# Kernel optimization log

Measured on AMD Instinct MI355X. Metric: run time of the kernel, lower is better.

## Reference

```python
import jax, jax.numpy as jnp
import numpy as np

DIM = 768
HEADS = 12
DIM_HEAD = DIM // HEADS  # 64
INNER = DIM_HEAD * HEADS  # 768
HIDDEN = 4 * DIM  # 3072
N = 31  # num_patches + 1, fixed by Block (num_patches=30)
B = 512
EPS = 1e-5
MASK_VAL = -987654321.0


def layernorm(x, g, b):
    mu = jnp.mean(x, axis=-1, keepdims=True)
    var = jnp.mean(jnp.square(x - mu), axis=-1, keepdims=True)
    return (x - mu) * jax.lax.rsqrt(var + EPS) * g + b


def setup_inputs() -> dict:
    key = jax.random.key(0)
    ks = jax.random.split(key, 12)
    s = 0.02
    return {
        "x": jax.random.normal(ks[0], (B, N, DIM), jnp.float32),
        "ln1_g": jnp.ones((DIM,), jnp.float32),
        "ln1_b": jnp.zeros((DIM,), jnp.float32),
        "w_qkv": jax.random.normal(ks[1], (DIM, 3 * INNER), jnp.float32) * s,
        "scale": jnp.full((HEADS,), DIM_HEAD ** -0.5, jnp.float32),
        "w_o": jax.random.normal(ks[2], (INNER, DIM), jnp.float32) * s,
        "b_o": jnp.zeros((DIM,), jnp.float32),
        "ln2_g": jnp.ones((DIM,), jnp.float32),
        "ln2_b": jnp.zeros((DIM,), jnp.float32),
        "w1": jax.random.normal(ks[3], (DIM, HIDDEN), jnp.float32) * s,
        "b1": jnp.zeros((HIDDEN,), jnp.float32),
        "w2": jax.random.normal(ks[4], (HIDDEN, DIM), jnp.float32) * s,
        "b2": jnp.zeros((DIM,), jnp.float32),
    }


def reference(x, ln1_g, ln1_b, w_qkv, scale, w_o, b_o, ln2_g, ln2_b, w1, b1, w2, b2):
    b, n, _ = x.shape
    # --- LSA attention ---
    h = layernorm(x, ln1_g, ln1_b)
    qkv = h @ w_qkv  # [b, n, 3*inner]
    q, k, v = jnp.split(qkv, 3, axis=-1)
    def split_heads(t):
        return t.reshape(b, n, HEADS, DIM_HEAD).transpose(0, 2, 1, 3)  # b h n d
    q, k, v = split_heads(q), split_heads(k), split_heads(v)
    dots = jnp.einsum('bhid,bhjd->bhij', q, k) * scale[None, :, None, None]
    # diagonal exclusion mask (self-token masked out)
    diag = jnp.eye(n, dtype=bool)
    dots = jnp.where(diag[None, None], MASK_VAL, dots)
    attn = jax.nn.softmax(dots, axis=-1)
    out = jnp.einsum('bhij,bhjd->bhid', attn, v)
    out = out.transpose(0, 2, 1, 3).reshape(b, n, INNER)
    x = x + out @ w_o + b_o
    # --- MLP ---
    h2 = layernorm(x, ln2_g, ln2_b)
    h2 = jax.nn.gelu(h2 @ w1 + b1, approximate=False)
    x = x + h2 @ w2 + b2
    return x
```

## Files before the change

### kernel.cpp

```cpp
#include <hip/hip_runtime.h>
#include <math.h>

#define DIM 768
#define HEADS 12
#define DHEAD 64
#define NTOK 31
#define BATCH 512
#define MTOK (BATCH * NTOK)
#define HIDDEN 3072
#define QKVN 2304
#define MASK_VAL -987654321.0f

typedef short s16x8 __attribute__((ext_vector_type(8)));
typedef float f32x4 __attribute__((ext_vector_type(4)));

static __device__ __forceinline__ float bs2f(unsigned short u) {
  unsigned int x = ((unsigned int)u) << 16;
  return __builtin_bit_cast(float, x);
}
static __device__ __forceinline__ unsigned short f2bs(float f) {
  unsigned int x = __builtin_bit_cast(unsigned int, f);
  x += 0x7fffu + ((x >> 16) & 1u);
  return (unsigned short)(x >> 16);
}

static __device__ __forceinline__ void gload16(const unsigned short* g, unsigned short* l) {
  __builtin_amdgcn_global_load_lds(
      (const __attribute__((address_space(1))) unsigned int*)g,
      (__attribute__((address_space(3))) unsigned int*)l, 16, 0, 0);
}

static __device__ __forceinline__ float epi_apply(int EPI, float v, int col, size_t idx,
                                                  const float* bias, const void* resid) {
  if (EPI == 0) return v;
  if (EPI == 2) {
    float t = v + bias[col];
    float arg = 1.5957691216f * t * (1.f + 0.044715f * t * t);
    return t * __builtin_amdgcn_rcpf(1.f + __expf(-arg));
  }
  if (EPI == 3) return v + bias[col] + ((const float*)resid)[idx];
  return v + bias[col] + bs2f(((const unsigned short*)resid)[idx]);
}

static __device__ __forceinline__ void epi_store(int EPI, void* outp, size_t idx, float t) {
  if (EPI == 4) ((float*)outp)[idx] = t;
  else ((unsigned short*)outp)[idx] = f2bs(t);
}

__global__ __launch_bounds__(256) void transpose_all_kernel(
    const float* __restrict__ w_qkv, const float* __restrict__ w_o,
    const float* __restrict__ w1, const float* __restrict__ w2,
    unsigned short* __restrict__ wqkvT, unsigned short* __restrict__ woT,
    unsigned short* __restrict__ w1T, unsigned short* __restrict__ w2T) {
  int t = blockIdx.x;
  const float* w;
  unsigned short* wt;
  int K, N, tx;
  if (t < 432) { w = w_qkv; wt = wqkvT; K = DIM; N = QKVN; tx = QKVN / 64; }
  else if (t < 576) { t -= 432; w = w_o; wt = woT; K = DIM; N = DIM; tx = DIM / 64; }
  else if (t < 1152) { t -= 576; w = w1; wt = w1T; K = DIM; N = HIDDEN; tx = HIDDEN / 64; }
  else { t -= 1152; w = w2; wt = w2T; K = HIDDEN; N = DIM; tx = DIM / 64; }
  int n0 = (t % tx) * 64, k0 = (t / tx) * 64;

  __shared__ float tl[64][65];
  int tid = threadIdx.x;
  int r = tid >> 4, c4 = (tid & 15) * 4;
#pragma unroll
  for (int i = 0; i < 4; ++i) {
    float4 v = *(const float4*)(w + (size_t)(k0 + r + i * 16) * N + n0 + c4);
    tl[r + i * 16][c4] = v.x;
    tl[r + i * 16][c4 + 1] = v.y;
    tl[r + i * 16][c4 + 2] = v.z;
    tl[r + i * 16][c4 + 3] = v.w;
  }
  __syncthreads();
#pragma unroll
  for (int i = 0; i < 4; ++i) {
    int n = r + i * 16;
    ushort4 o;
    o.x = f2bs(tl[c4 + 0][n]);
    o.y = f2bs(tl[c4 + 1][n]);
    o.z = f2bs(tl[c4 + 2][n]);
    o.w = f2bs(tl[c4 + 3][n]);
    *(ushort4*)(wt + (size_t)(n0 + n) * K + k0 + c4) = o;
  }
}

__global__ __launch_bounds__(256) void ln_kernel(const float* __restrict__ x,
                                                 const float* __restrict__ g,
                                                 const float* __restrict__ bta,
                                                 unsigned short* __restrict__ out) {
  int wid = threadIdx.x >> 6, lane = threadIdx.x & 63;
  size_t row = (size_t)blockIdx.x * 4 + wid;
  const float4* xr = (const float4*)(x + row * DIM);
  float4 v[3];
  v[0] = xr[lane];
  v[1] = xr[lane + 64];
  v[2] = xr[lane + 128];
  float s = 0.f, sq = 0.f;
#pragma unroll
  for (int i = 0; i < 3; ++i) {
    s += v[i].x + v[i].y + v[i].z + v[i].w;
    sq += v[i].x * v[i].x + v[i].y * v[i].y + v[i].z * v[i].z + v[i].w * v[i].w;
  }
#pragma unroll
  for (int off = 32; off; off >>= 1) {
    s += __shfl_xor(s, off);
    sq += __shfl_xor(sq, off);
  }
  float mu = s * (1.f / DIM);
  float var = sq * (1.f / DIM) - mu * mu;
  float rs = rsqrtf(var + 1e-5f);
#pragma unroll
  for (int i = 0; i < 3; ++i) {
    int col = i * 256 + lane * 4;
    float4 gg = *(const float4*)(g + col);
    float4 bb = *(const float4*)(bta + col);
    ushort4 o;
    o.x = f2bs((v[i].x - mu) * rs * gg.x + bb.x);
    o.y = f2bs((v[i].y - mu) * rs * gg.y + bb.y);
    o.z = f2bs((v[i].z - mu) * rs * gg.z + bb.z);
    o.w = f2bs((v[i].w - mu) * rs * gg.w + bb.w);
    *(ushort4*)(out + row * DIM + col) = o;
  }
}

__global__ __launch_bounds__(256) void ln_bf16_kernel(const unsigned short* __restrict__ x,
                                                      const float* __restrict__ g,
                                                      const float* __restrict__ bta,
                                                      unsigned short* __restrict__ out) {
  int wid = threadIdx.x >> 6, lane = threadIdx.x & 63;
  size_t row = (size_t)blockIdx.x * 4 + wid;
  const unsigned short* xr = x + row * DIM;
  float v[12];
#pragma unroll
  for (int i = 0; i < 3; ++i) {
    ushort4 u = *(const ushort4*)(xr + i * 256 + lane * 4);
    v[i * 4 + 0] = bs2f(u.x);
    v[i * 4 + 1] = bs2f(u.y);
    v[i * 4 + 2] = bs2f(u.z);
    v[i * 4 + 3] = bs2f(u.w);
  }
  float s = 0.f, sq = 0.f;
#pragma unroll
  for (int i = 0; i < 12; ++i) {
    s += v[i];
    sq += v[i] * v[i];
  }
#pragma unroll
  for (int off = 32; off; off >>= 1) {
    s += __shfl_xor(s, off);
    sq += __shfl_xor(sq, off);
  }
  float mu = s * (1.f / DIM);
  float var = sq * (1.f / DIM) - mu * mu;
  float rs = rsqrtf(var + 1e-5f);
#pragma unroll
  for (int i = 0; i < 3; ++i) {
    int col = i * 256 + lane * 4;
    float4 gg = *(const float4*)(g + col);
    float4 bb = *(const float4*)(bta + col);
    ushort4 o;
    o.x = f2bs((v[i * 4 + 0] - mu) * rs * gg.x + bb.x);
    o.y = f2bs((v[i * 4 + 1] - mu) * rs * gg.y + bb.y);
    o.z = f2bs((v[i * 4 + 2] - mu) * rs * gg.z + bb.z);
    o.w = f2bs((v[i * 4 + 3] - mu) * rs * gg.w + bb.w);
    *(ushort4*)(out + row * DIM + col) = o;
  }
}

template <int AB, int BB, int VM, typename STF>
__device__ __forceinline__ void gphm(const char* aBase, const char* bBase,
                                     f32x4 (&acc)[4][4], STF&& stage) {
  const char* aP = aBase + AB * 8192;
  const char* bP = bBase + BB * 16384;
  s16x8 af[4], bk[4];
#pragma unroll
  for (int ni = 0; ni < 4; ++ni) bk[ni] = *(const s16x8*)(bP + ni * 1024);
#pragma unroll
  for (int mi = 0; mi < 4; ++mi) af[mi] = *(const s16x8*)(aP + mi * 1024);
  stage();
  if (VM == 2) asm volatile("s_waitcnt vmcnt(2)");
  if (VM == 0) asm volatile("s_waitcnt vmcnt(0)");
  __builtin_amdgcn_s_barrier();
  asm volatile("s_waitcnt lgkmcnt(0)");
  __builtin_amdgcn_s_setprio(1);
#pragma unroll
  for (int mi = 0; mi < 4; ++mi)
#pragma unroll
    for (int ni = 0; ni < 4; ++ni)
      acc[mi][ni] =
          __builtin_amdgcn_mfma_f32_16x16x32_bf16(af[mi], bk[ni], acc[mi][ni], 0, 0, 0);
  __builtin_amdgcn_s_setprio(0);
  __builtin_amdgcn_s_barrier();
}

template <int EPI>
__device__ __forceinline__ void gemm128m_body(
    const unsigned short* __restrict__ A, const unsigned short* __restrict__ Bt,
    void* __restrict__ outp, const float* __restrict__ bias,
    const void* __restrict__ resid, int M, int N, int K, int ntn) {
  __shared__ char ldsc[65536];
  int tid = threadIdx.x;
  int lane = tid & 63, w = tid >> 6;
  int wm = w >> 2, wn = w & 3;
  int fr = lane & 15, q = lane >> 4;

  int nwg = gridDim.x, orig = blockIdx.x;
  int qd = nwg >> 3, r8 = nwg & 7, xcd = orig & 7, loc = orig >> 3;
  int bid = (xcd < r8 ? xcd * (qd + 1) : r8 * (qd + 1) + (xcd - r8) * qd) + loc;
  int m0 = (bid / ntn) * 128, n0 = (bid % ntn) * 256;

  int rdoff = (q * 16) ^ (((fr >> 1) & 3) << 4);
  const char* aBase = ldsc + (wm * 64 + fr) * 64 + rdoff;
  const char* bBase = ldsc + 16384 + (wn * 64 + fr) * 64 + rdoff;

  int srow = tid >> 2;
  int seoff = (((tid & 3) ^ ((srow >> 1) & 3))) << 3;
  const char* Ab = (const char*)A + ((size_t)(m0 + srow) * K + seoff) * 2;
  const char* Bb = (const char*)Bt + ((size_t)(n0 + srow) * K + seoff) * 2;
  size_t rstep = (size_t)K * 256;

  auto stgA = [&](int buf, int tile) {
    gload16((const unsigned short*)(Ab + tile * 64),
            (unsigned short*)(ldsc + buf * 8192 + w * 1024));
  };
  auto stgB = [&](int buf, int tile) {
    const char* gp = Bb + tile * 64;
    char* lp = ldsc + 16384 + buf * 16384 + w * 1024;
    gload16((const unsigned short*)gp, (unsigned short*)lp);
    gload16((const unsigned short*)(gp + rstep), (unsigned short*)(lp + 8192));
  };
  auto nop = [&] {};

  f32x4 acc[4][4] = {};
  stgA(0, 0);
  stgB(0, 0);
  stgB(1, 1);
  asm volatile("s_waitcnt vmcnt(2)");
  __builtin_amdgcn_s_barrier();

#pragma unroll 1
  for (int T = 0; T < 18; T += 6) {
    gphm<0, 0, 2>(aBase, bBase, acc, [&] { stgA(1, T + 1); stgB(2, T + 2); });
    gphm<1, 1, 2>(aBase, bBase, acc, [&] { stgA(0, T + 2); stgB(0, T + 3); });
    gphm<0, 2, 2>(aBase, bBase, acc, [&] { stgA(1, T + 3); stgB(1, T + 4); });
    gphm<1, 0, 2>(aBase, bBase, acc, [&] { stgA(0, T + 4); stgB(2, T + 5); });
    gphm<0, 1, 2>(aBase, bBase, acc, [&] { stgA(1, T + 5); stgB(0, T + 6); });
    gphm<1, 2, 2>(aBase, bBase, acc, [&] { stgA(0, T + 6); stgB(1, T + 7); });
  }
  gphm<0, 0, 2>(aBase, bBase, acc, [&] { stgA(1, 19); stgB(2, 20); });
  gphm<1, 1, 2>(aBase, bBase, acc, [&] { stgA(0, 20); stgB(0, 21); });
  gphm<0, 2, 2>(aBase, bBase, acc, [&] { stgA(1, 21); stgB(1, 22); });
  gphm<1, 0, 2>(aBase, bBase, acc, [&] { stgA(0, 22); stgB(2, 23); });
  gphm<0, 1, 0>(aBase, bBase, acc, [&] { stgA(1, 23); });
  gphm<1, 2, -1>(aBase, bBase, acc, nop);

#pragma unroll
  for (int am = 0; am < 4; ++am)
#pragma unroll
    for (int ni = 0; ni < 4; ++ni)
#pragma unroll
      for (int rr = 0; rr < 4; ++rr) {
        int row = m0 + wm * 64 + am * 16 + q * 4 + rr;
        int col = n0 + wn * 64 + ni * 16 + fr;
        size_t idx = (size_t)row * N + col;
        epi_store(EPI, outp, idx, epi_apply(EPI, acc[am][ni][rr], col, idx, bias, resid));
      }
}

template <int BUF, int MH, int KH, int VM, typename STF>
__device__ __forceinline__ void gph192(const char* aB0, const char* bKH0, const char* bKH1,
                                       s16x8 (&bk)[3], f32x4 (&acc)[8][3], STF&& stage) {
  const char* aP = aB0 + BUF * 32768 + KH * 16384 + MH * 4096;
  s16x8 af[4];
  if (MH == 0) {
    const char* bp = (KH ? bKH1 : bKH0) + BUF * 24576;
#pragma unroll
    for (int ni = 0; ni < 3; ++ni) bk[ni] = *(const s16x8*)(bp + ni * 2048);
  }
#pragma unroll
  for (int mi = 0; mi < 4; ++mi) af[mi] = *(const s16x8*)(aP + mi * 1024);
  stage();
  if (VM == 2) asm volatile("s_waitcnt vmcnt(2)");
  if (VM == 0) asm volatile("s_waitcnt vmcnt(0)");
  __builtin_amdgcn_s_barrier();
  asm volatile("s_waitcnt lgkmcnt(0)");
  __builtin_amdgcn_s_setprio(1);
#pragma unroll
  for (int mi = 0; mi < 4; ++mi)
#pragma unroll
    for (int ni = 0; ni < 3; ++ni)
      acc[MH * 4 + mi][ni] =
          __builtin_amdgcn_mfma_f32_16x16x32_bf16(af[mi], bk[ni], acc[MH * 4 + mi][ni], 0, 0, 0);
  __builtin_amdgcn_s_setprio(0);
  __builtin_amdgcn_s_barrier();
}

template <int EPI>
__device__ __forceinline__ void gemm192_body(
    const unsigned short* __restrict__ A, const unsigned short* __restrict__ Bt,
    void* __restrict__ outp, const float* __restrict__ bias,
    const void* __restrict__ resid, int M, int N, int K, int ntn) {
  __shared__ char ldsc[114688];
  int tid = threadIdx.x;
  int lane = tid & 63, w = tid >> 6;
  int wm = w >> 2, wn = w & 3;
  int fr = lane & 15, q = lane >> 4;

  int nwg = gridDim.x, orig = blockIdx.x;
  int qd = nwg >> 3, r8 = nwg & 7, xcd = orig & 7, loc = orig >> 3;
  int bid = (xcd < r8 ? xcd * (qd + 1) : r8 * (qd + 1) + (xcd - r8) * qd) + loc;
  int m0 = (bid / ntn) * 256, n0 = (bid % ntn) * 192;

  int rdoffA = (q * 16) ^ (((fr >> 1) & 3) << 4);
  const char* aB0 = ldsc + (wm * 128 + fr) * 64 + rdoffA;
  int brow0 = wn * 48 + fr;
  int bsw = brow0 & 7;
  const char* bBase = ldsc + 65536 + brow0 * 128 + (q ^ (bsw & 3)) * 16;
  const char* bKH0 = bBase + ((0 ^ (bsw >> 2)) * 64);
  const char* bKH1 = bBase + ((1 ^ (bsw >> 2)) * 64);

  int srow = tid >> 2;
  int seoffA = (((tid & 3) ^ ((srow >> 1) & 3))) << 3;
  const char* Ab = (const char*)A + ((size_t)(m0 + srow) * K + seoffA) * 2;
  size_t rstep = (size_t)K * 256;
  auto stgA = [&](int kh, int buf, int tile) {
    const char* gp = Ab + tile * 128 + kh * 64;
    unsigned short* lp = (unsigned short*)(ldsc + buf * 32768 + kh * 16384 + w * 1024);
    gload16((const unsigned short*)gp, lp);
    gload16((const unsigned short*)(gp + rstep), (unsigned short*)((char*)lp + 8192));
  };
  const char* Bb2 = (const char*)Bt +
                    ((size_t)(n0 + (tid >> 3)) * K + (((tid & 7) ^ ((tid >> 3) & 7)) * 8)) * 2;
  auto stgB = [&](int j, int buf, int tile) {
    gload16((const unsigned short*)(Bb2 + (size_t)j * 128 * K + tile * 128),
            (unsigned short*)(ldsc + 65536 + buf * 24576 + j * 8192 + w * 1024));
  };
  auto nop = [&] {};

  f32x4 acc[8][3] = {};
  s16x8 bk[3];
  int NT = K / 64;

  stgA(0, 0, 0);
  stgA(1, 0, 0);
  stgB(0, 0, 0);
  stgB(1, 0, 0);
  stgB(2, 0, 0);
  stgA(0, 1, 1);
  asm volatile("s_waitcnt vmcnt(2)");
  __builtin_amdgcn_s_barrier();

  for (int t = 0; t + 3 < NT; t += 2) {
    gph192<0, 0, 0, -1>(aB0, bKH0, bKH1, bk, acc,
                        [&] { stgA(1, 1, t + 1); stgB(0, 1, t + 1); stgB(1, 1, t + 1); });
    gph192<0, 1, 0, -1>(aB0, bKH0, bKH1, bk, acc, [&] { stgB(2, 1, t + 1); });
    gph192<0, 0, 1, -1>(aB0, bKH0, bKH1, bk, acc, [&] { stgA(0, 0, t + 2); });
    gph192<0, 1, 1, 2>(aB0, bKH0, bKH1, bk, acc, nop);
    gph192<1, 0, 0, -1>(aB0, bKH0, bKH1, bk, acc,
                        [&] { stgA(1, 0, t + 2); stgB(0, 0, t + 2); stgB(1, 0, t + 2); });
    gph192<1, 1, 0, -1>(aB0, bKH0, bKH1, bk, acc, [&] { stgB(2, 0, t + 2); });
    gph192<1, 0, 1, -1>(aB0, bKH0, bKH1, bk, acc, [&] { stgA(0, 1, t + 3); });
    gph192<1, 1, 1, 2>(aB0, bKH0, bKH1, bk, acc, nop);
  }
  gph192<0, 0, 0, -1>(aB0, bKH0, bKH1, bk, acc,
                      [&] { stgA(1, 1, NT - 1); stgB(0, 1, NT - 1); stgB(1, 1, NT - 1); });
  gph192<0, 1, 0, -1>(aB0, bKH0, bKH1, bk, acc, [&] { stgB(2, 1, NT - 1); });
  gph192<0, 0, 1, -1>(aB0, bKH0, bKH1, bk, acc, nop);
  gph192<0, 1, 1, 0>(aB0, bKH0, bKH1, bk, acc, nop);
  gph192<1, 0, 0, -1>(aB0, bKH0, bKH1, bk, acc, nop);
  gph192<1, 1, 0, -1>(aB0, bKH0, bKH1, bk, acc, nop);
  gph192<1, 0, 1, -1>(aB0, bKH0, bKH1, bk, acc, nop);
  gph192<1, 1, 1, -1>(aB0, bKH0, bKH1, bk, acc, nop);

#pragma unroll
  for (int am = 0; am < 8; ++am)
#pragma unroll
    for (int ni = 0; ni < 3; ++ni)
#pragma unroll
      for (int rr = 0; rr < 4; ++rr) {
        int row = m0 + wm * 128 + am * 16 + q * 4 + rr;
        int col = n0 + wn * 48 + ni * 16 + fr;
        size_t idx = (size_t)row * N + col;
        epi_store(EPI, outp, idx, epi_apply(EPI, acc[am][ni][rr], col, idx, bias, resid));
      }
}

__global__ __launch_bounds__(512, 4) void gemm_qkv(const unsigned short* A,
                                                   const unsigned short* Bt, void* o,
                                                   const float* b, const void* r, int M,
                                                   int N, int K, int ntn) {
  gemm128m_body<0>(A, Bt, o, b, r, M, N, K, ntn);
}
__global__ __launch_bounds__(512, 4) void gemm_mlp1(const unsigned short* A,
                                                    const unsigned short* Bt, void* o,
                                                    const float* b, const void* r, int M,
                                                    int N, int K, int ntn) {
  gemm128m_body<2>(A, Bt, o, b, r, M, N, K, ntn);
}
__global__ __launch_bounds__(512, 2) void gemm_proj(const unsigned short* A,
                                                    const unsigned short* Bt, void* o,
                                                    const float* b, const void* r, int M,
                                                    int N, int K, int ntn) {
  gemm192_body<3>(A, Bt, o, b, r, M, N, K, ntn);
}
__global__ __launch_bounds__(512, 2) void gemm_mlp2(const unsigned short* A,
                                                    const unsigned short* Bt, void* o,
                                                    const float* b, const void* r, int M,
                                                    int N, int K, int ntn) {
  gemm192_body<4>(A, Bt, o, b, r, M, N, K, ntn);
}

__global__ __launch_bounds__(256) void attn_mfma_kernel(const unsigned short* __restrict__ qkv,
                                                        const float* __restrict__ scale,
                                                        unsigned short* __restrict__ ao) {
  __shared__ unsigned short Vt[4][64][40];
  __shared__ unsigned short Pl[4][32][32];
  int wid = threadIdx.x >> 6, lane = threadIdx.x & 63;
  int pair = blockIdx.x * 4 + wid;
  int b = pair / HEADS, h = pair % HEADS;
  const unsigned short* base = qkv + (size_t)b * NTOK * QKVN + h * DHEAD;
  const unsigned short* Qp = base;
  const unsigned short* Kp = base + 768;
  const unsigned short* Vp = base + 1536;

  int c = lane & 15, q = lane >> 4;
  int oct = q * 8;

  unsigned short vcol[NTOK];
#pragma unroll
  for (int j = 0; j < NTOK; ++j) vcol[j] = Vp[(size_t)j * QKVN + lane];
#pragma unroll
  for (int j = 0; j < NTOK; ++j) Vt[wid][lane][j] = vcol[j];
  Vt[wid][lane][31] = 0;

  s16x8 kf[2][2] = {{{0}}}, qf[2][2] = {{{0}}};
#pragma unroll
  for (int t = 0; t < 2; ++t) {
    int row = t * 16 + c;
    if (row < NTOK) {
#pragma unroll
      for (int s = 0; s < 2; ++s) {
        kf[t][s] = *(const s16x8*)(Kp + (size_t)row * QKVN + s * 32 + oct);
        qf[t][s] = *(const s16x8*)(Qp + (size_t)row * QKVN + s * 32 + oct);
      }
    }
  }

  f32x4 st[2][2] = {};
#pragma unroll
  for (int jt = 0; jt < 2; ++jt)
#pragma unroll
    for (int it = 0; it < 2; ++it)
#pragma unroll
      for (int s = 0; s < 2; ++s)
        st[jt][it] =
            __builtin_amdgcn_mfma_f32_16x16x32_bf16(kf[jt][s], qf[it][s], st[jt][it], 0, 0, 0);

  float scl = scale[h];
  float p[2][2][4];
#pragma unroll
  for (int it = 0; it < 2; ++it)
#pragma unroll
    for (int jt = 0; jt < 2; ++jt)
#pragma unroll
      for (int r = 0; r < 4; ++r) {
        int j = jt * 16 + 4 * q + r;
        int i = it * 16 + c;
        float v = st[jt][it][r] * scl;
        if (j == 31 || j == i) v = MASK_VAL;
        p[it][jt][r] = v;
      }
#pragma unroll
  for (int it = 0; it < 2; ++it) {
    float m = p[it][0][0];
#pragma unroll
    for (int jt = 0; jt < 2; ++jt)
#pragma unroll
      for (int r = 0; r < 4; ++r) m = fmaxf(m, p[it][jt][r]);
    m = fmaxf(m, __shfl_xor(m, 16));
    m = fmaxf(m, __shfl_xor(m, 32));
    float s = 0.f;
#pragma unroll
    for (int jt = 0; jt < 2; ++jt)
#pragma unroll
      for (int r = 0; r < 4; ++r) {
        float e = __expf(p[it][jt][r] - m);
        p[it][jt][r] = e;
        s += e;
      }
    s += __shfl_xor(s, 16);
    s += __shfl_xor(s, 32);
    float inv = __builtin_amdgcn_rcpf(s);
#pragma unroll
    for (int jt = 0; jt < 2; ++jt)
#pragma unroll
      for (int r = 0; r < 4; ++r) p[it][jt][r] *= inv;
  }
#pragma unroll
  for (int it = 0; it < 2; ++it)
#pragma unroll
    for (int jt = 0; jt < 2; ++jt) {
      unsigned int w0 =
          (unsigned int)f2bs(p[it][jt][0]) | ((unsigned int)f2bs(p[it][jt][1]) << 16);
      unsigned int w1 =
          (unsigned int)f2bs(p[it][jt][2]) | ((unsigned int)f2bs(p[it][jt][3]) << 16);
      uint2 pk = {w0, w1};
      *(uint2*)&Pl[wid][it * 16 + c][jt * 16 + 4 * q] = pk;
    }

  s16x8 pa[2];
#pragma unroll
  for (int it = 0; it < 2; ++it) pa[it] = *(const s16x8*)&Pl[wid][it * 16 + c][oct];
  f32x4 o[2][4];
#pragma unroll
  for (int it = 0; it < 2; ++it)
#pragma unroll
    for (int dt = 0; dt < 4; ++dt) {
      s16x8 vb = *(const s16x8*)&Vt[wid][dt * 16 + c][oct];
      f32x4 z = {0.f, 0.f, 0.f, 0.f};
      o[it][dt] = __builtin_amdgcn_mfma_f32_16x16x32_bf16(pa[it], vb, z, 0, 0, 0);
    }
#pragma unroll
  for (int it = 0; it < 2; ++it)
#pragma unroll
    for (int r = 0; r < 4; ++r) {
      int i = it * 16 + 4 * q + r;
      if (i < NTOK) {
        size_t rowoff = ((size_t)b * NTOK + i) * DIM + h * DHEAD;
#pragma unroll
        for (int dt = 0; dt < 4; ++dt) ao[rowoff + dt * 16 + c] = f2bs(o[it][dt][r]);
      }
    }
}

extern "C" void kernel_launch(void* const* d_in, const int* in_sizes, int n_in,
                              void* d_out, int out_size, void* d_ws, size_t ws_size,
                              hipStream_t stream) {
  (void)in_sizes; (void)n_in; (void)out_size; (void)ws_size;
  const float* x = (const float*)d_in[0];
  const float* ln1_g = (const float*)d_in[1];
  const float* ln1_b = (const float*)d_in[2];
  const float* w_qkv = (const float*)d_in[3];
  const float* scale = (const float*)d_in[4];
  const float* w_o = (const float*)d_in[5];
  const float* b_o = (const float*)d_in[6];
  const float* ln2_g = (const float*)d_in[7];
  const float* ln2_b = (const float*)d_in[8];
  const float* w1 = (const float*)d_in[9];
  const float* b1 = (const float*)d_in[10];
  const float* w2 = (const float*)d_in[11];
  const float* b2 = (const float*)d_in[12];

  char* ws = (char*)d_ws;
  unsigned short* buf1 = (unsigned short*)(ws + 0);
  unsigned short* qkv_bf = (unsigned short*)(ws + 24379392);
  unsigned short* x2 = (unsigned short*)(ws + 24379392);
  unsigned short* g_bf = (unsigned short*)(ws + 97517568);
  unsigned short* wqkvT = (unsigned short*)(ws + 195035136);
  unsigned short* woT = (unsigned short*)(ws + 198574080);
  unsigned short* w1T = (unsigned short*)(ws + 199753728);
  unsigned short* w2T = (unsigned short*)(ws + 204472320);

  transpose_all_kernel<<<1728, 256, 0, stream>>>(w_qkv, w_o, w1, w2, wqkvT, woT, w1T, w2T);

  ln_kernel<<<MTOK / 4, 256, 0, stream>>>(x, ln1_g, ln1_b, buf1);
  gemm_qkv<<<(MTOK / 128) * (QKVN / 256), 512, 0, stream>>>(
      buf1, wqkvT, qkv_bf, nullptr, nullptr, MTOK, QKVN, DIM, QKVN / 256);
  attn_mfma_kernel<<<(BATCH * HEADS) / 4, 256, 0, stream>>>(qkv_bf, scale, buf1);
  gemm_proj<<<(MTOK / 256) * (DIM / 192), 512, 0, stream>>>(
      buf1, woT, x2, b_o, x, MTOK, DIM, DIM, DIM / 192);
  ln_bf16_kernel<<<MTOK / 4, 256, 0, stream>>>(x2, ln2_g, ln2_b, buf1);
  gemm_mlp1<<<(MTOK / 128) * (HIDDEN / 256), 512, 0, stream>>>(
      buf1, w1T, g_bf, b1, nullptr, MTOK, HIDDEN, DIM, HIDDEN / 256);
  gemm_mlp2<<<(MTOK / 256) * (DIM / 192), 512, 0, stream>>>(
      g_bf, w2T, (float*)d_out, b2, x2, MTOK, DIM, HIDDEN, DIM / 192);
}
```

Baseline: 323.7 us.

## Load B fragments directly to registers from pre-tiled weight layout in QKV/MLP1 GEMMs

```diff
diff --git a/kernel.cpp b/kernel.cpp
--- a/kernel.cpp
+++ b/kernel.cpp
@@ -30,6 +30,12 @@
       (__attribute__((address_space(3))) unsigned int*)l, 16, 0, 0);
 }
 
+static __device__ __forceinline__ s16x8 gload_reg(const char* p) {
+  s16x8 r;
+  asm volatile("global_load_dwordx4 %0, %1, off" : "=v"(r) : "v"(p));
+  return r;
+}
+
 static __device__ __forceinline__ float epi_apply(int EPI, float v, int col, size_t idx,
                                                   const float* bias, const void* resid) {
   if (EPI == 0) return v;
@@ -55,11 +61,11 @@
   int t = blockIdx.x;
   const float* w;
   unsigned short* wt;
-  int K, N, tx;
-  if (t < 432) { w = w_qkv; wt = wqkvT; K = DIM; N = QKVN; tx = QKVN / 64; }
-  else if (t < 576) { t -= 432; w = w_o; wt = woT; K = DIM; N = DIM; tx = DIM / 64; }
-  else if (t < 1152) { t -= 576; w = w1; wt = w1T; K = DIM; N = HIDDEN; tx = HIDDEN / 64; }
-  else { t -= 1152; w = w2; wt = w2T; K = HIDDEN; N = DIM; tx = DIM / 64; }
+  int K, N, tx, tiled;
+  if (t < 432) { w = w_qkv; wt = wqkvT; K = DIM; N = QKVN; tx = QKVN / 64; tiled = 1; }
+  else if (t < 576) { t -= 432; w = w_o; wt = woT; K = DIM; N = DIM; tx = DIM / 64; tiled = 0; }
+  else if (t < 1152) { t -= 576; w = w1; wt = w1T; K = DIM; N = HIDDEN; tx = HIDDEN / 64; tiled = 1; }
+  else { t -= 1152; w = w2; wt = w2T; K = HIDDEN; N = DIM; tx = DIM / 64; tiled = 0; }
   int n0 = (t % tx) * 64, k0 = (t / tx) * 64;
 
   __shared__ float tl[64][65];
@@ -82,7 +88,13 @@
     o.y = f2bs(tl[c4 + 1][n]);
     o.z = f2bs(tl[c4 + 2][n]);
     o.w = f2bs(tl[c4 + 3][n]);
-    *(ushort4*)(wt + (size_t)(n0 + n) * K + k0 + c4) = o;
+    if (tiled) {
+      size_t si = ((size_t)((n0 + n) >> 4) * (K >> 3) + ((k0 + c4) >> 3)) * 128 +
+                  (n & 15) * 8 + (c4 & 7);
+      *(ushort4*)(wt + si) = o;
+    } else {
+      *(ushort4*)(wt + (size_t)(n0 + n) * K + k0 + c4) = o;
+    }
   }
 }
 
@@ -169,38 +181,39 @@
   }
 }
 
-template <int AB, int BB, int VM, typename STF>
-__device__ __forceinline__ void gphm(const char* aBase, const char* bBase,
-                                     f32x4 (&acc)[4][4], STF&& stage) {
-  const char* aP = aBase + AB * 8192;
-  const char* bP = bBase + BB * 16384;
-  s16x8 af[4], bk[4];
-#pragma unroll
-  for (int ni = 0; ni < 4; ++ni) bk[ni] = *(const s16x8*)(bP + ni * 1024);
-#pragma unroll
-  for (int mi = 0; mi < 4; ++mi) af[mi] = *(const s16x8*)(aP + mi * 1024);
-  stage();
-  if (VM == 2) asm volatile("s_waitcnt vmcnt(2)");
+template <int ABUF, int BSEL, int VM, typename SA, typename SB>
+__device__ __forceinline__ void gphd(const char* aBase, s16x8 (&bk)[2][4],
+                                     f32x4 (&acc)[4][4], SA&& stageA, SB&& loadB) {
+  stageA();
+  s16x8 af[4];
+#pragma unroll
+  for (int mi = 0; mi < 4; ++mi)
+    af[mi] = *(const s16x8*)(aBase + ABUF * 8192 + mi * 1024);
+  if (VM == 5) asm volatile("s_waitcnt vmcnt(5)");
+  if (VM == 4) asm volatile("s_waitcnt vmcnt(4)");
   if (VM == 0) asm volatile("s_waitcnt vmcnt(0)");
   __builtin_amdgcn_s_barrier();
   asm volatile("s_waitcnt lgkmcnt(0)");
+  __builtin_amdgcn_sched_barrier(0);
   __builtin_amdgcn_s_setprio(1);
 #pragma unroll
   for (int mi = 0; mi < 4; ++mi)
 #pragma unroll
     for (int ni = 0; ni < 4; ++ni)
       acc[mi][ni] =
-          __builtin_amdgcn_mfma_f32_16x16x32_bf16(af[mi], bk[ni], acc[mi][ni], 0, 0, 0);
+          __builtin_amdgcn_mfma_f32_16x16x32_bf16(af[mi], bk[BSEL][ni], acc[mi][ni], 0, 0, 0);
   __builtin_amdgcn_s_setprio(0);
+  loadB();
   __builtin_amdgcn_s_barrier();
 }
 
 template <int EPI>
-__device__ __forceinline__ void gemm128m_body(
+__device__ __forceinline__ void gemm128d_body(
     const unsigned short* __restrict__ A, const unsigned short* __restrict__ Bt,
     void* __restrict__ outp, const float* __restrict__ bias,
-    const void* __restrict__ resid, int M, int N, int K, int ntn) {
-  __shared__ char ldsc[65536];
+    const void* __restrict__ resid, int M, int N, int ntn) {
+  constexpr int K = 768;
+  __shared__ char ldsc[24576];
   int tid = threadIdx.x;
   int lane = tid & 63, w = tid >> 6;
   int wm = w >> 2, wn = w & 3;
@@ -213,48 +226,47 @@
 
   int rdoff = (q * 16) ^ (((fr >> 1) & 3) << 4);
   const char* aBase = ldsc + (wm * 64 + fr) * 64 + rdoff;
-  const char* bBase = ldsc + 16384 + (wn * 64 + fr) * 64 + rdoff;
 
   int srow = tid >> 2;
   int seoff = (((tid & 3) ^ ((srow >> 1) & 3))) << 3;
   const char* Ab = (const char*)A + ((size_t)(m0 + srow) * K + seoff) * 2;
-  const char* Bb = (const char*)Bt + ((size_t)(n0 + srow) * K + seoff) * 2;
-  size_t rstep = (size_t)K * 256;
+
+  const char* bB[4];
+#pragma unroll
+  for (int ni = 0; ni < 4; ++ni)
+    bB[ni] = (const char*)Bt +
+             ((size_t)((n0 + wn * 64 + ni * 16) >> 4) * (K >> 3) + q) * 256 + fr * 16;
 
   auto stgA = [&](int buf, int tile) {
     gload16((const unsigned short*)(Ab + tile * 64),
             (unsigned short*)(ldsc + buf * 8192 + w * 1024));
   };
-  auto stgB = [&](int buf, int tile) {
-    const char* gp = Bb + tile * 64;
-    char* lp = ldsc + 16384 + buf * 16384 + w * 1024;
-    gload16((const unsigned short*)gp, (unsigned short*)lp);
-    gload16((const unsigned short*)(gp + rstep), (unsigned short*)(lp + 8192));
+  s16x8 bk[2][4];
+  auto loadB = [&](int sel, int tile) {
+#pragma unroll
+    for (int ni = 0; ni < 4; ++ni) bk[sel][ni] = gload_reg(bB[ni] + (size_t)tile * 1024);
   };
-  auto nop = [&] {};
 
   f32x4 acc[4][4] = {};
+
   stgA(0, 0);
-  stgB(0, 0);
-  stgB(1, 1);
-  asm volatile("s_waitcnt vmcnt(2)");
+  stgA(1, 1);
+  loadB(0, 0);
+  loadB(1, 1);
+  asm volatile("s_waitcnt vmcnt(8)");
   __builtin_amdgcn_s_barrier();
 
-#pragma unroll 1
-  for (int T = 0; T < 18; T += 6) {
-    gphm<0, 0, 2>(aBase, bBase, acc, [&] { stgA(1, T + 1); stgB(2, T + 2); });
-    gphm<1, 1, 2>(aBase, bBase, acc, [&] { stgA(0, T + 2); stgB(0, T + 3); });
-    gphm<0, 2, 2>(aBase, bBase, acc, [&] { stgA(1, T + 3); stgB(1, T + 4); });
-    gphm<1, 0, 2>(aBase, bBase, acc, [&] { stgA(0, T + 4); stgB(2, T + 5); });
-    gphm<0, 1, 2>(aBase, bBase, acc, [&] { stgA(1, T + 5); stgB(0, T + 6); });
-    gphm<1, 2, 2>(aBase, bBase, acc, [&] { stgA(0, T + 6); stgB(1, T + 7); });
-  }
-  gphm<0, 0, 2>(aBase, bBase, acc, [&] { stgA(1, 19); stgB(2, 20); });
-  gphm<1, 1, 2>(aBase, bBase, acc, [&] { stgA(0, 20); stgB(0, 21); });
-  gphm<0, 2, 2>(aBase, bBase, acc, [&] { stgA(1, 21); stgB(1, 22); });
-  gphm<1, 0, 2>(aBase, bBase, acc, [&] { stgA(0, 22); stgB(2, 23); });
-  gphm<0, 1, 0>(aBase, bBase, acc, [&] { stgA(1, 23); });
-  gphm<1, 2, -1>(aBase, bBase, acc, nop);
+#define PH(p) gphd<(p) % 3, (p) & 1, 5>(aBase, bk, acc, \
+      [&] { stgA(((p) + 2) % 3, (p) + 2); }, [&] { loadB((p) & 1, (p) + 2); })
+  PH(0); PH(1); PH(2); PH(3); PH(4); PH(5);
+  PH(6); PH(7); PH(8); PH(9); PH(10); PH(11);
+  PH(12); PH(13); PH(14); PH(15); PH(16); PH(17);
+  PH(18); PH(19); PH(20); PH(21);
+#undef PH
+  auto nopA = [&] {};
+  auto nopB = [&] {};
+  gphd<22 % 3, 0, 4>(aBase, bk, acc, nopA, nopB);
+  gphd<23 % 3, 1, 0>(aBase, bk, acc, nopA, nopB);
 
 #pragma unroll
   for (int am = 0; am < 4; ++am)
@@ -387,17 +399,17 @@
       }
 }
 
-__global__ __launch_bounds__(512, 4) void gemm_qkv(const unsigned short* A,
+__global__ __launch_bounds__(512, 2) void gemm_qkv(const unsigned short* A,
                                                    const unsigned short* Bt, void* o,
                                                    const float* b, const void* r, int M,
-                                                   int N, int K, int ntn) {
-  gemm128m_body<0>(A, Bt, o, b, r, M, N, K, ntn);
-}
-__global__ __launch_bounds__(512, 4) void gemm_mlp1(const unsigned short* A,
+                                                   int N, int ntn) {
+  gemm128d_body<0>(A, Bt, o, b, r, M, N, ntn);
+}
+__global__ __launch_bounds__(512, 2) void gemm_mlp1(const unsigned short* A,
                                                     const unsigned short* Bt, void* o,
                                                     const float* b, const void* r, int M,
-                                                    int N, int K, int ntn) {
-  gemm128m_body<2>(A, Bt, o, b, r, M, N, K, ntn);
+                                                    int N, int ntn) {
+  gemm128d_body<2>(A, Bt, o, b, r, M, N, ntn);
 }
 __global__ __launch_bounds__(512, 2) void gemm_proj(const unsigned short* A,
                                                     const unsigned short* Bt, void* o,
@@ -567,13 +579,13 @@
 
   ln_kernel<<<MTOK / 4, 256, 0, stream>>>(x, ln1_g, ln1_b, buf1);
   gemm_qkv<<<(MTOK / 128) * (QKVN / 256), 512, 0, stream>>>(
-      buf1, wqkvT, qkv_bf, nullptr, nullptr, MTOK, QKVN, DIM, QKVN / 256);
+      buf1, wqkvT, qkv_bf, nullptr, nullptr, MTOK, QKVN, QKVN / 256);
   attn_mfma_kernel<<<(BATCH * HEADS) / 4, 256, 0, stream>>>(qkv_bf, scale, buf1);
   gemm_proj<<<(MTOK / 256) * (DIM / 192), 512, 0, stream>>>(
       buf1, woT, x2, b_o, x, MTOK, DIM, DIM, DIM / 192);
   ln_bf16_kernel<<<MTOK / 4, 256, 0, stream>>>(x2, ln2_g, ln2_b, buf1);
   gemm_mlp1<<<(MTOK / 128) * (HIDDEN / 256), 512, 0, stream>>>(
-      buf1, w1T, g_bf, b1, nullptr, MTOK, HIDDEN, DIM, HIDDEN / 256);
+      buf1, w1T, g_bf, b1, nullptr, MTOK, HIDDEN, HIDDEN / 256);
   gemm_mlp2<<<(MTOK / 256) * (DIM / 192), 512, 0, stream>>>(
       g_bf, w2T, (float*)d_out, b2, x2, MTOK, DIM, HIDDEN, DIM / 192);
 }
```

Result: no change. 320.8 us (-0.9%).

## Use 256x192 tile GEMM for all projections with multiple tiles per block

Applied to the files above, without the earlier changes.

```diff
diff --git a/kernel.cpp b/kernel.cpp
--- a/kernel.cpp
+++ b/kernel.cpp
@@ -169,14 +169,16 @@
   }
 }
 
-template <int AB, int BB, int VM, typename STF>
-__device__ __forceinline__ void gphm(const char* aBase, const char* bBase,
-                                     f32x4 (&acc)[4][4], STF&& stage) {
-  const char* aP = aBase + AB * 8192;
-  const char* bP = bBase + BB * 16384;
-  s16x8 af[4], bk[4];
-#pragma unroll
-  for (int ni = 0; ni < 4; ++ni) bk[ni] = *(const s16x8*)(bP + ni * 1024);
+template <int BUF, int MH, int KH, int VM, typename STF>
+__device__ __forceinline__ void gph192(const char* aB0, const char* bKH0, const char* bKH1,
+                                       s16x8 (&bk)[3], f32x4 (&acc)[8][3], STF&& stage) {
+  const char* aP = aB0 + BUF * 32768 + KH * 16384 + MH * 4096;
+  s16x8 af[4];
+  if (MH == 0) {
+    const char* bp = (KH ? bKH1 : bKH0) + BUF * 24576;
+#pragma unroll
+    for (int ni = 0; ni < 3; ++ni) bk[ni] = *(const s16x8*)(bp + ni * 2048);
+  }
 #pragma unroll
   for (int mi = 0; mi < 4; ++mi) af[mi] = *(const s16x8*)(aP + mi * 1024);
   stage();
@@ -188,108 +190,6 @@
 #pragma unroll
   for (int mi = 0; mi < 4; ++mi)
 #pragma unroll
-    for (int ni = 0; ni < 4; ++ni)
-      acc[mi][ni] =
-          __builtin_amdgcn_mfma_f32_16x16x32_bf16(af[mi], bk[ni], acc[mi][ni], 0, 0, 0);
-  __builtin_amdgcn_s_setprio(0);
-  __builtin_amdgcn_s_barrier();
-}
-
-template <int EPI>
-__device__ __forceinline__ void gemm128m_body(
-    const unsigned short* __restrict__ A, const unsigned short* __restrict__ Bt,
-    void* __restrict__ outp, const float* __restrict__ bias,
-    const void* __restrict__ resid, int M, int N, int K, int ntn) {
-  __shared__ char ldsc[65536];
-  int tid = threadIdx.x;
-  int lane = tid & 63, w = tid >> 6;
-  int wm = w >> 2, wn = w & 3;
-  int fr = lane & 15, q = lane >> 4;
-
-  int nwg = gridDim.x, orig = blockIdx.x;
-  int qd = nwg >> 3, r8 = nwg & 7, xcd = orig & 7, loc = orig >> 3;
-  int bid = (xcd < r8 ? xcd * (qd + 1) : r8 * (qd + 1) + (xcd - r8) * qd) + loc;
-  int m0 = (bid / ntn) * 128, n0 = (bid % ntn) * 256;
-
-  int rdoff = (q * 16) ^ (((fr >> 1) & 3) << 4);
-  const char* aBase = ldsc + (wm * 64 + fr) * 64 + rdoff;
-  const char* bBase = ldsc + 16384 + (wn * 64 + fr) * 64 + rdoff;
-
-  int srow = tid >> 2;
-  int seoff = (((tid & 3) ^ ((srow >> 1) & 3))) << 3;
-  const char* Ab = (const char*)A + ((size_t)(m0 + srow) * K + seoff) * 2;
-  const char* Bb = (const char*)Bt + ((size_t)(n0 + srow) * K + seoff) * 2;
-  size_t rstep = (size_t)K * 256;
-
-  auto stgA = [&](int buf, int tile) {
-    gload16((const unsigned short*)(Ab + tile * 64),
-            (unsigned short*)(ldsc + buf * 8192 + w * 1024));
-  };
-  auto stgB = [&](int buf, int tile) {
-    const char* gp = Bb + tile * 64;
-    char* lp = ldsc + 16384 + buf * 16384 + w * 1024;
-    gload16((const unsigned short*)gp, (unsigned short*)lp);
-    gload16((const unsigned short*)(gp + rstep), (unsigned short*)(lp + 8192));
-  };
-  auto nop = [&] {};
-
-  f32x4 acc[4][4] = {};
-  stgA(0, 0);
-  stgB(0, 0);
-  stgB(1, 1);
-  asm volatile("s_waitcnt vmcnt(2)");
-  __builtin_amdgcn_s_barrier();
-
-#pragma unroll 1
-  for (int T = 0; T < 18; T += 6) {
-    gphm<0, 0, 2>(aBase, bBase, acc, [&] { stgA(1, T + 1); stgB(2, T + 2); });
-    gphm<1, 1, 2>(aBase, bBase, acc, [&] { stgA(0, T + 2); stgB(0, T + 3); });
-    gphm<0, 2, 2>(aBase, bBase, acc, [&] { stgA(1, T + 3); stgB(1, T + 4); });
-    gphm<1, 0, 2>(aBase, bBase, acc, [&] { stgA(0, T + 4); stgB(2, T + 5); });
-    gphm<0, 1, 2>(aBase, bBase, acc, [&] { stgA(1, T + 5); stgB(0, T + 6); });
-    gphm<1, 2, 2>(aBase, bBase, acc, [&] { stgA(0, T + 6); stgB(1, T + 7); });
-  }
-  gphm<0, 0, 2>(aBase, bBase, acc, [&] { stgA(1, 19); stgB(2, 20); });
-  gphm<1, 1, 2>(aBase, bBase, acc, [&] { stgA(0, 20); stgB(0, 21); });
-  gphm<0, 2, 2>(aBase, bBase, acc, [&] { stgA(1, 21); stgB(1, 22); });
-  gphm<1, 0, 2>(aBase, bBase, acc, [&] { stgA(0, 22); stgB(2, 23); });
-  gphm<0, 1, 0>(aBase, bBase, acc, [&] { stgA(1, 23); });
-  gphm<1, 2, -1>(aBase, bBase, acc, nop);
-
-#pragma unroll
-  for (int am = 0; am < 4; ++am)
-#pragma unroll
-    for (int ni = 0; ni < 4; ++ni)
-#pragma unroll
-      for (int rr = 0; rr < 4; ++rr) {
-        int row = m0 + wm * 64 + am * 16 + q * 4 + rr;
-        int col = n0 + wn * 64 + ni * 16 + fr;
-        size_t idx = (size_t)row * N + col;
-        epi_store(EPI, outp, idx, epi_apply(EPI, acc[am][ni][rr], col, idx, bias, resid));
-      }
-}
-
-template <int BUF, int MH, int KH, int VM, typename STF>
-__device__ __forceinline__ void gph192(const char* aB0, const char* bKH0, const char* bKH1,
-                                       s16x8 (&bk)[3], f32x4 (&acc)[8][3], STF&& stage) {
-  const char* aP = aB0 + BUF * 32768 + KH * 16384 + MH * 4096;
-  s16x8 af[4];
-  if (MH == 0) {
-    const char* bp = (KH ? bKH1 : bKH0) + BUF * 24576;
-#pragma unroll
-    for (int ni = 0; ni < 3; ++ni) bk[ni] = *(const s16x8*)(bp + ni * 2048);
-  }
-#pragma unroll
-  for (int mi = 0; mi < 4; ++mi) af[mi] = *(const s16x8*)(aP + mi * 1024);
-  stage();
-  if (VM == 2) asm volatile("s_waitcnt vmcnt(2)");
-  if (VM == 0) asm volatile("s_waitcnt vmcnt(0)");
-  __builtin_amdgcn_s_barrier();
-  asm volatile("s_waitcnt lgkmcnt(0)");
-  __builtin_amdgcn_s_setprio(1);
-#pragma unroll
-  for (int mi = 0; mi < 4; ++mi)
-#pragma unroll
     for (int ni = 0; ni < 3; ++ni)
       acc[MH * 4 + mi][ni] =
           __builtin_amdgcn_mfma_f32_16x16x32_bf16(af[mi], bk[ni], acc[MH * 4 + mi][ni], 0, 0, 0);
@@ -297,7 +197,7 @@
   __builtin_amdgcn_s_barrier();
 }
 
-template <int EPI>
+template <int EPI, int TPB>
 __device__ __forceinline__ void gemm192_body(
     const unsigned short* __restrict__ A, const unsigned short* __restrict__ Bt,
     void* __restrict__ outp, const float* __restrict__ bias,
@@ -311,7 +211,6 @@
   int nwg = gridDim.x, orig = blockIdx.x;
   int qd = nwg >> 3, r8 = nwg & 7, xcd = orig & 7, loc = orig >> 3;
   int bid = (xcd < r8 ? xcd * (qd + 1) : r8 * (qd + 1) + (xcd - r8) * qd) + loc;
-  int m0 = (bid / ntn) * 256, n0 = (bid % ntn) * 192;
 
   int rdoffA = (q * 16) ^ (((fr >> 1) & 3) << 4);
   const char* aB0 = ldsc + (wm * 128 + fr) * 64 + rdoffA;
@@ -323,93 +222,101 @@
 
   int srow = tid >> 2;
   int seoffA = (((tid & 3) ^ ((srow >> 1) & 3))) << 3;
-  const char* Ab = (const char*)A + ((size_t)(m0 + srow) * K + seoffA) * 2;
   size_t rstep = (size_t)K * 256;
-  auto stgA = [&](int kh, int buf, int tile) {
-    const char* gp = Ab + tile * 128 + kh * 64;
-    unsigned short* lp = (unsigned short*)(ldsc + buf * 32768 + kh * 16384 + w * 1024);
-    gload16((const unsigned short*)gp, lp);
-    gload16((const unsigned short*)(gp + rstep), (unsigned short*)((char*)lp + 8192));
-  };
-  const char* Bb2 = (const char*)Bt +
-                    ((size_t)(n0 + (tid >> 3)) * K + (((tid & 7) ^ ((tid >> 3) & 7)) * 8)) * 2;
-  auto stgB = [&](int j, int buf, int tile) {
-    gload16((const unsigned short*)(Bb2 + (size_t)j * 128 * K + tile * 128),
-            (unsigned short*)(ldsc + 65536 + buf * 24576 + j * 8192 + w * 1024));
-  };
-  auto nop = [&] {};
-
-  f32x4 acc[8][3] = {};
-  s16x8 bk[3];
   int NT = K / 64;
 
-  stgA(0, 0, 0);
-  stgA(1, 0, 0);
-  stgB(0, 0, 0);
-  stgB(1, 0, 0);
-  stgB(2, 0, 0);
-  stgA(0, 1, 1);
-  asm volatile("s_waitcnt vmcnt(2)");
-  __builtin_amdgcn_s_barrier();
-
-  for (int t = 0; t + 3 < NT; t += 2) {
+#pragma unroll 1
+  for (int tl = 0; tl < TPB; ++tl) {
+    int tile = bid * TPB + tl;
+    int m0 = (tile / ntn) * 256, n0 = (tile % ntn) * 192;
+
+    const char* Ab = (const char*)A + ((size_t)(m0 + srow) * K + seoffA) * 2;
+    const char* Bb2 = (const char*)Bt +
+        ((size_t)(n0 + (tid >> 3)) * K + (((tid & 7) ^ ((tid >> 3) & 7)) * 8)) * 2;
+
+    auto stgA = [&](int kh, int buf, int t) {
+      const char* gp = Ab + t * 128 + kh * 64;
+      unsigned short* lp = (unsigned short*)(ldsc + buf * 32768 + kh * 16384 + w * 1024);
+      gload16((const unsigned short*)gp, lp);
+      gload16((const unsigned short*)(gp + rstep), (unsigned short*)((char*)lp + 8192));
+    };
+    auto stgB = [&](int j, int buf, int t) {
+      gload16((const unsigned short*)(Bb2 + (size_t)j * 128 * K + t * 128),
+              (unsigned short*)(ldsc + 65536 + buf * 24576 + j * 8192 + w * 1024));
+    };
+    auto nop = [&] {};
+
+    f32x4 acc[8][3] = {};
+    s16x8 bk[3];
+
+    stgA(0, 0, 0);
+    stgA(1, 0, 0);
+    stgB(0, 0, 0);
+    stgB(1, 0, 0);
+    stgB(2, 0, 0);
+    stgA(0, 1, 1);
+    asm volatile("s_waitcnt vmcnt(2)");
+    __builtin_amdgcn_s_barrier();
+
+    for (int t = 0; t + 3 < NT; t += 2) {
+      gph192<0, 0, 0, -1>(aB0, bKH0, bKH1, bk, acc,
+                          [&] { stgA(1, 1, t + 1); stgB(0, 1, t + 1); stgB(1, 1, t + 1); });
+      gph192<0, 1, 0, -1>(aB0, bKH0, bKH1, bk, acc, [&] { stgB(2, 1, t + 1); });
+      gph192<0, 0, 1, -1>(aB0, bKH0, bKH1, bk, acc, [&] { stgA(0, 0, t + 2); });
+      gph192<0, 1, 1, 2>(aB0, bKH0, bKH1, bk, acc, nop);
+      gph192<1, 0, 0, -1>(aB0, bKH0, bKH1, bk, acc,
+                          [&] { stgA(1, 0, t + 2); stgB(0, 0, t + 2); stgB(1, 0, t + 2); });
+      gph192<1, 1, 0, -1>(aB0, bKH0, bKH1, bk, acc, [&] { stgB(2, 0, t + 2); });
+      gph192<1, 0, 1, -1>(aB0, bKH0, bKH1, bk, acc, [&] { stgA(0, 1, t + 3); });
+      gph192<1, 1, 1, 2>(aB0, bKH0, bKH1, bk, acc, nop);
+    }
     gph192<0, 0, 0, -1>(aB0, bKH0, bKH1, bk, acc,
-                        [&] { stgA(1, 1, t + 1); stgB(0, 1, t + 1); stgB(1, 1, t + 1); });
-    gph192<0, 1, 0, -1>(aB0, bKH0, bKH1, bk, acc, [&] { stgB(2, 1, t + 1); });
-    gph192<0, 0, 1, -1>(aB0, bKH0, bKH1, bk, acc, [&] { stgA(0, 0, t + 2); });
-    gph192<0, 1, 1, 2>(aB0, bKH0, bKH1, bk, acc, nop);
-    gph192<1, 0, 0, -1>(aB0, bKH0, bKH1, bk, acc,
-                        [&] { stgA(1, 0, t + 2); stgB(0, 0, t + 2); stgB(1, 0, t + 2); });
-    gph192<1, 1, 0, -1>(aB0, bKH0, bKH1, bk, acc, [&] { stgB(2, 0, t + 2); });
-    gph192<1, 0, 1, -1>(aB0, bKH0, bKH1, bk, acc, [&] { stgA(0, 1, t + 3); });
-    gph192<1, 1, 1, 2>(aB0, bKH0, bKH1, bk, acc, nop);
-  }
-  gph192<0, 0, 0, -1>(aB0, bKH0, bKH1, bk, acc,
-                      [&] { stgA(1, 1, NT - 1); stgB(0, 1, NT - 1); stgB(1, 1, NT - 1); });
-  gph192<0, 1, 0, -1>(aB0, bKH0, bKH1, bk, acc, [&] { stgB(2, 1, NT - 1); });
-  gph192<0, 0, 1, -1>(aB0, bKH0, bKH1, bk, acc, nop);
-  gph192<0, 1, 1, 0>(aB0, bKH0, bKH1, bk, acc, nop);
-  gph192<1, 0, 0, -1>(aB0, bKH0, bKH1, bk, acc, nop);
-  gph192<1, 1, 0, -1>(aB0, bKH0, bKH1, bk, acc, nop);
-  gph192<1, 0, 1, -1>(aB0, bKH0, bKH1, bk, acc, nop);
-  gph192<1, 1, 1, -1>(aB0, bKH0, bKH1, bk, acc, nop);
-
-#pragma unroll
-  for (int am = 0; am < 8; ++am)
-#pragma unroll
-    for (int ni = 0; ni < 3; ++ni)
-#pragma unroll
-      for (int rr = 0; rr < 4; ++rr) {
-        int row = m0 + wm * 128 + am * 16 + q * 4 + rr;
-        int col = n0 + wn * 48 + ni * 16 + fr;
-        size_t idx = (size_t)row * N + col;
-        epi_store(EPI, outp, idx, epi_apply(EPI, acc[am][ni][rr], col, idx, bias, resid));
-      }
-}
-
-__global__ __launch_bounds__(512, 4) void gemm_qkv(const unsigned short* A,
+                        [&] { stgA(1, 1, NT - 1); stgB(0, 1, NT - 1); stgB(1, 1, NT - 1); });
+    gph192<0, 1, 0, -1>(aB0, bKH0, bKH1, bk, acc, [&] { stgB(2, 1, NT - 1); });
+    gph192<0, 0, 1, -1>(aB0, bKH0, bKH1, bk, acc, nop);
+    gph192<0, 1, 1, 0>(aB0, bKH0, bKH1, bk, acc, nop);
+    gph192<1, 0, 0, -1>(aB0, bKH0, bKH1, bk, acc, nop);
+    gph192<1, 1, 0, -1>(aB0, bKH0, bKH1, bk, acc, nop);
+    gph192<1, 0, 1, -1>(aB0, bKH0, bKH1, bk, acc, nop);
+    gph192<1, 1, 1, -1>(aB0, bKH0, bKH1, bk, acc, nop);
+
+#pragma unroll
+    for (int am = 0; am < 8; ++am)
+#pragma unroll
+      for (int ni = 0; ni < 3; ++ni)
+#pragma unroll
+        for (int rr = 0; rr < 4; ++rr) {
+          int row = m0 + wm * 128 + am * 16 + q * 4 + rr;
+          int col = n0 + wn * 48 + ni * 16 + fr;
+          size_t idx = (size_t)row * N + col;
+          epi_store(EPI, outp, idx, epi_apply(EPI, acc[am][ni][rr], col, idx, bias, resid));
+        }
+  }
+}
+
+__global__ __launch_bounds__(512, 2) void gemm_qkv(const unsigned short* A,
                                                    const unsigned short* Bt, void* o,
                                                    const float* b, const void* r, int M,
                                                    int N, int K, int ntn) {
-  gemm128m_body<0>(A, Bt, o, b, r, M, N, K, ntn);
-}
-__global__ __launch_bounds__(512, 4) void gemm_mlp1(const unsigned short* A,
+  gemm192_body<0, 3>(A, Bt, o, b, r, M, N, K, ntn);
+}
+__global__ __launch_bounds__(512, 2) void gemm_mlp1(const unsigned short* A,
                                                     const unsigned short* Bt, void* o,
                                                     const float* b, const void* r, int M,
                                                     int N, int K, int ntn) {
-  gemm128m_body<2>(A, Bt, o, b, r, M, N, K, ntn);
+  gemm192_body<2, 4>(A, Bt, o, b, r, M, N, K, ntn);
 }
 __global__ __launch_bounds__(512, 2) void gemm_proj(const unsigned short* A,
                                                     const unsigned short* Bt, void* o,
                                                     const float* b, const void* r, int M,
                                                     int N, int K, int ntn) {
-  gemm192_body<3>(A, Bt, o, b, r, M, N, K, ntn);
+  gemm192_body<3, 1>(A, Bt, o, b, r, M, N, K, ntn);
 }
 __global__ __launch_bounds__(512, 2) void gemm_mlp2(const unsigned short* A,
                                                     const unsigned short* Bt, void* o,
                                                     const float* b, const void* r, int M,
                                                     int N, int K, int ntn) {
-  gemm192_body<4>(A, Bt, o, b, r, M, N, K, ntn);
+  gemm192_body<4, 1>(A, Bt, o, b, r, M, N, K, ntn);
 }
 
 __global__ __launch_bounds__(256) void attn_mfma_kernel(const unsigned short* __restrict__ qkv,
@@ -566,14 +473,14 @@
   transpose_all_kernel<<<1728, 256, 0, stream>>>(w_qkv, w_o, w1, w2, wqkvT, woT, w1T, w2T);
 
   ln_kernel<<<MTOK / 4, 256, 0, stream>>>(x, ln1_g, ln1_b, buf1);
-  gemm_qkv<<<(MTOK / 128) * (QKVN / 256), 512, 0, stream>>>(
-      buf1, wqkvT, qkv_bf, nullptr, nullptr, MTOK, QKVN, DIM, QKVN / 256);
+  gemm_qkv<<<248, 512, 0, stream>>>(
+      buf1, wqkvT, qkv_bf, nullptr, nullptr, MTOK, QKVN, DIM, QKVN / 192);
   attn_mfma_kernel<<<(BATCH * HEADS) / 4, 256, 0, stream>>>(qkv_bf, scale, buf1);
-  gemm_proj<<<(MTOK / 256) * (DIM / 192), 512, 0, stream>>>(
+  gemm_proj<<<248, 512, 0, stream>>>(
       buf1, woT, x2, b_o, x, MTOK, DIM, DIM, DIM / 192);
   ln_bf16_kernel<<<MTOK / 4, 256, 0, stream>>>(x2, ln2_g, ln2_b, buf1);
-  gemm_mlp1<<<(MTOK / 128) * (HIDDEN / 256), 512, 0, stream>>>(
-      buf1, w1T, g_bf, b1, nullptr, MTOK, HIDDEN, DIM, HIDDEN / 256);
-  gemm_mlp2<<<(MTOK / 256) * (DIM / 192), 512, 0, stream>>>(
+  gemm_mlp1<<<248, 512, 0, stream>>>(
+      buf1, w1T, g_bf, b1, nullptr, MTOK, HIDDEN, DIM, HIDDEN / 192);
+  gemm_mlp2<<<248, 512, 0, stream>>>(
       g_bf, w2T, (float*)d_out, b2, x2, MTOK, DIM, HIDDEN, DIM / 192);
 }
```

Result: faster. 313.2 us (-3.2%).
